# Optimization experiments

Measured on AMD Instinct MI355X. Metric: run time of the kernel, lower is better.

The kernel has to match this reference:

```python
import jax, jax.numpy as jnp
import numpy as np

B, S, D = 8, 2048, 256


def setup_inputs() -> dict:
    key = jax.random.key(0)
    kq, kk, kv, km = jax.random.split(key, 4)
    q = jax.random.normal(kq, (B, S, D), dtype=jnp.float32)
    k = jax.random.normal(kk, (B, S, D), dtype=jnp.float32)
    v = jax.random.normal(kv, (B, S, D), dtype=jnp.float32)
    mask = jax.random.randint(km, (B, S, S), 0, 2, dtype=jnp.int32)
    return {"q": q, "k": k, "v": v, "mask": mask}


def reference(q, k, v, mask):
    d_k = q.shape[-1]
    scale = 1.0 / jnp.sqrt(jnp.float32(d_k))
    # scores: [B, S, S]
    attn = jnp.einsum('bqd,bkd->bqk', q, k) * scale
    attn = jnp.where(mask == 0, jnp.float32(-1e9), attn)
    attn = jax.nn.softmax(attn, axis=-1)
    out = jnp.einsum('bqk,bkd->bqd', attn, v)
    return (out, attn)
```

## Files before the change

### kernel.cpp

```cpp
#include <hip/hip_runtime.h>

constexpr int B = 8, S = 2048, D = 256;
constexpr int TQ = 32;
constexpr float SCALE = 0.0625f;
constexpr int PSTRIDE = 2056;

typedef __attribute__((ext_vector_type(8))) short bf16x8;
typedef __attribute__((ext_vector_type(4))) float f32x4;

__device__ __forceinline__ short f2bf(float f) {
    union { float f; unsigned u; } c; c.f = f;
    unsigned u = c.u + 0x7fffu + ((c.u >> 16) & 1u);
    return (short)(u >> 16);
}

__global__ __launch_bounds__(256) void prepass(
    const float* __restrict__ k, const float* __restrict__ v,
    short* __restrict__ kb, short* __restrict__ vtb)
{
    __shared__ float tile[64][65];
    const int blk = blockIdx.x;
    const int tid = threadIdx.x;

    if (blk < 4096) {
        int i = blk * 256 + tid;
        float4 x = ((const float4*)k)[i];
        short4 o; o.x = f2bf(x.x); o.y = f2bf(x.y); o.z = f2bf(x.z); o.w = f2bf(x.w);
        ((short4*)kb)[i] = o;
    } else {
        int blk2 = blk - 4096;
        int b = blk2 >> 7, rem = blk2 & 127;
        int d0 = (rem & 3) * 64, k0 = (rem >> 2) * 64;
        int tr = tid >> 4, tc = tid & 15;
        const float* vb = v + (size_t)b * S * D;
        #pragma unroll
        for (int r = 0; r < 4; ++r) {
            int key = r * 16 + tr;
            float4 x = *(const float4*)(vb + (size_t)(k0 + key) * D + d0 + tc * 4);
            tile[key][tc * 4 + 0] = x.x; tile[key][tc * 4 + 1] = x.y;
            tile[key][tc * 4 + 2] = x.z; tile[key][tc * 4 + 3] = x.w;
        }
        __syncthreads();
        short* vtbb = vtb + (size_t)b * D * S;
        #pragma unroll
        for (int r = 0; r < 4; ++r) {
            int d = r * 16 + tr;
            short4 o;
            o.x = f2bf(tile[tc * 4 + 0][d]); o.y = f2bf(tile[tc * 4 + 1][d]);
            o.z = f2bf(tile[tc * 4 + 2][d]); o.w = f2bf(tile[tc * 4 + 3][d]);
            *(short4*)(vtbb + (size_t)(d0 + d) * S + k0 + tc * 4) = o;
        }
    }
}

__global__ __launch_bounds__(512, 2) void attn_mfma(
    const float* __restrict__ qf, const short* __restrict__ kb,
    const short* __restrict__ vtb, const int* __restrict__ maskg,
    float* __restrict__ outg, float* __restrict__ attng)
{
    const int b = blockIdx.x & 7;
    const int i0 = (blockIdx.x >> 3) * TQ;
    const int tid = threadIdx.x;
    const int wave = tid >> 6, lane = tid & 63;
    const int quad = lane >> 4, l16 = lane & 15;

    __shared__ short p_lds[TQ][PSTRIDE];
    __shared__ float red[8][TQ];

    bf16x8 aq[2][8];
    const float* qbase = qf + ((size_t)b * S + i0) * D;
    #pragma unroll
    for (int mt = 0; mt < 2; ++mt)
        #pragma unroll
        for (int ks = 0; ks < 8; ++ks) {
            const float* p = qbase + (size_t)(mt * 16 + l16) * D + ks * 32 + quad * 8;
            float4 x0 = *(const float4*)p;
            float4 x1 = *(const float4*)(p + 4);
            bf16x8 a;
            a[0] = f2bf(x0.x); a[1] = f2bf(x0.y); a[2] = f2bf(x0.z); a[3] = f2bf(x0.w);
            a[4] = f2bf(x1.x); a[5] = f2bf(x1.y); a[6] = f2bf(x1.z); a[7] = f2bf(x1.w);
            aq[mt][ks] = a;
        }

    f32x4 acc[2][16];
    #pragma unroll
    for (int mt = 0; mt < 2; ++mt)
        #pragma unroll
        for (int nt = 0; nt < 16; ++nt)
            acc[mt][nt] = f32x4{0.f, 0.f, 0.f, 0.f};

    float rsum[2] = {0.f, 0.f};
    const short* kbase = kb + (size_t)b * S * D;
    const int* mbase0 = maskg + ((size_t)b * S + i0 + l16) * S + wave * 256 + quad * 4;
    const int* mbase1 = mbase0 + (size_t)16 * S;

    #pragma unroll
    for (int nt = 0; nt < 16; ++nt) {
        const int n0 = wave * 256 + nt * 16;
        int4 m0 = *(const int4*)(mbase0 + nt * 16);
        int4 m1 = *(const int4*)(mbase1 + nt * 16);
        bf16x8 bk[8];
        #pragma unroll
        for (int ks = 0; ks < 8; ++ks)
            bk[ks] = *(const bf16x8*)(kbase + (size_t)(n0 + l16) * D + ks * 32 + quad * 8);
        #pragma unroll
        for (int ks = 0; ks < 8; ++ks) {
            acc[0][nt] = __builtin_amdgcn_mfma_f32_16x16x32_bf16(bk[ks], aq[0][ks], acc[0][nt], 0, 0, 0);
            acc[1][nt] = __builtin_amdgcn_mfma_f32_16x16x32_bf16(bk[ks], aq[1][ks], acc[1][nt], 0, 0, 0);
        }
        const int mm0[4] = {m0.x, m0.y, m0.z, m0.w};
        const int mm1[4] = {m1.x, m1.y, m1.z, m1.w};
        #pragma unroll
        for (int r = 0; r < 4; ++r) {
            float e0 = mm0[r] ? __expf(acc[0][nt][r] * SCALE) : 0.0f;
            acc[0][nt][r] = e0; rsum[0] += e0;
            float e1 = mm1[r] ? __expf(acc[1][nt][r] * SCALE) : 0.0f;
            acc[1][nt][r] = e1; rsum[1] += e1;
        }
    }

    #pragma unroll
    for (int mt = 0; mt < 2; ++mt) {
        float v = rsum[mt];
        v += __shfl_xor(v, 16); v += __shfl_xor(v, 32);
        if (quad == 0) red[wave][mt * 16 + l16] = v;
    }
    __syncthreads();

    float inv[2];
    #pragma unroll
    for (int mt = 0; mt < 2; ++mt) {
        float tot = 0.f;
        #pragma unroll
        for (int w = 0; w < 8; ++w) tot += red[w][mt * 16 + l16];
        inv[mt] = 1.0f / tot;
    }

    #pragma unroll
    for (int mt = 0; mt < 2; ++mt) {
        float* arow = attng + ((size_t)b * S + i0 + mt * 16 + l16) * S + wave * 256 + quad * 4;
        #pragma unroll
        for (int nt = 0; nt < 16; ++nt) {
            float4 p4; short4 pb;
            float p0 = acc[mt][nt][0] * inv[mt];
            float p1 = acc[mt][nt][1] * inv[mt];
            float p2 = acc[mt][nt][2] * inv[mt];
            float p3 = acc[mt][nt][3] * inv[mt];
            p4.x = p0; p4.y = p1; p4.z = p2; p4.w = p3;
            pb.x = f2bf(p0); pb.y = f2bf(p1); pb.z = f2bf(p2); pb.w = f2bf(p3);
            *(float4*)(arow + nt * 16) = p4;
            *(short4*)&p_lds[mt * 16 + l16][wave * 256 + nt * 16 + quad * 4] = pb;
        }
    }

    asm volatile("s_waitcnt lgkmcnt(0)" ::: "memory");
    __builtin_amdgcn_s_barrier();
    asm volatile("" ::: "memory");

    f32x4 oacc[2][2];
    #pragma unroll
    for (int mt = 0; mt < 2; ++mt)
        #pragma unroll
        for (int nc = 0; nc < 2; ++nc) oacc[mt][nc] = f32x4{0.f, 0.f, 0.f, 0.f};

    const short* vbase = vtb + (size_t)b * D * S;
    const int nb = wave * 32;
    for (int ks = 0; ks < 64; ++ks) {
        bf16x8 ap[2], bv[2];
        #pragma unroll
        for (int mt = 0; mt < 2; ++mt)
            ap[mt] = *(const bf16x8*)&p_lds[mt * 16 + l16][ks * 32 + quad * 8];
        #pragma unroll
        for (int nc = 0; nc < 2; ++nc)
            bv[nc] = *(const bf16x8*)(vbase + (size_t)(nb + nc * 16 + l16) * S + ks * 32 + quad * 8);
        #pragma unroll
        for (int mt = 0; mt < 2; ++mt)
            #pragma unroll
            for (int nc = 0; nc < 2; ++nc)
                oacc[mt][nc] = __builtin_amdgcn_mfma_f32_16x16x32_bf16(ap[mt], bv[nc], oacc[mt][nc], 0, 0, 0);
    }

    #pragma unroll
    for (int mt = 0; mt < 2; ++mt)
        #pragma unroll
        for (int nc = 0; nc < 2; ++nc)
            #pragma unroll
            for (int r = 0; r < 4; ++r) {
                int row = i0 + mt * 16 + quad * 4 + r;
                int col = nb + nc * 16 + l16;
                outg[((size_t)b * S + row) * D + col] = oacc[mt][nc][r];
            }
}

extern "C" void kernel_launch(void* const* d_in, const int* in_sizes, int n_in,
                              void* d_out, int out_size, void* d_ws, size_t ws_size,
                              hipStream_t stream) {
    const float* q    = (const float*)d_in[0];
    const float* k    = (const float*)d_in[1];
    const float* v    = (const float*)d_in[2];
    const int*   mask = (const int*)d_in[3];
    float* out  = (float*)d_out;
    float* attn = out + (size_t)B * S * D;

    const size_t N = (size_t)B * S * D;
    short* kb  = (short*)d_ws;
    short* vtb = kb + N;

    prepass<<<dim3(5120), 256, 0, stream>>>(k, v, kb, vtb);
    attn_mfma<<<dim3((S / TQ) * B), 512, 0, stream>>>(q, kb, vtb, mask, out, attn);
}
```

Before: 412.6 us.

## Recompute QK^T in a second pass to cut registers and shrink the LDS tile

The large per-wave score accumulator array (32 f32x4) and the full 32x2048 bf16 probability tile in LDS are replaced by a two-pass scheme. The first pass computes QK^T in 256-key chunks, accumulates row sums and packs the mask into 64-bit bitmasks, without keeping the scores. The second pass recomputes QK^T per chunk, normalizes, writes attn, and stages a double-buffered 32x256 bf16 tile in LDS that feeds the PV MFMAs chunk by chunk. This lowers register and LDS use so launch bounds can target 4 blocks per CU, at the cost of doubling the QK^T MFMA work and K reads, plus one barrier per chunk.

```diff
diff --git a/kernel.cpp b/kernel.cpp
--- a/kernel.cpp
+++ b/kernel.cpp
@@ -3,7 +3,7 @@
 constexpr int B = 8, S = 2048, D = 256;
 constexpr int TQ = 32;
 constexpr float SCALE = 0.0625f;
-constexpr int PSTRIDE = 2056;
+constexpr int PST = 264;
 
 typedef __attribute__((ext_vector_type(8))) short bf16x8;
 typedef __attribute__((ext_vector_type(4))) float f32x4;
@@ -53,7 +53,7 @@
     }
 }
 
-__global__ __launch_bounds__(512, 2) void attn_mfma(
+__global__ __launch_bounds__(512, 4) void attn_mfma(
     const float* __restrict__ qf, const short* __restrict__ kb,
     const short* __restrict__ vtb, const int* __restrict__ maskg,
     float* __restrict__ outg, float* __restrict__ attng)
@@ -64,7 +64,7 @@
     const int wave = tid >> 6, lane = tid & 63;
     const int quad = lane >> 4, l16 = lane & 15;
 
-    __shared__ short p_lds[TQ][PSTRIDE];
+    __shared__ short p_lds[2][TQ][PST];
     __shared__ float red[8][TQ];
 
     bf16x8 aq[2][8];
@@ -82,41 +82,51 @@
             aq[mt][ks] = a;
         }
 
-    f32x4 acc[2][16];
-    #pragma unroll
-    for (int mt = 0; mt < 2; ++mt)
-        #pragma unroll
-        for (int nt = 0; nt < 16; ++nt)
-            acc[mt][nt] = f32x4{0.f, 0.f, 0.f, 0.f};
+    const short* kbase = kb + (size_t)b * S * D;
+    const int* mrow0 = maskg + ((size_t)b * S + i0 + l16) * S + quad * 4;
+    const int* mrow1 = mrow0 + (size_t)16 * S;
 
     float rsum[2] = {0.f, 0.f};
-    const short* kbase = kb + (size_t)b * S * D;
-    const int* mbase0 = maskg + ((size_t)b * S + i0 + l16) * S + wave * 256 + quad * 4;
-    const int* mbase1 = mbase0 + (size_t)16 * S;
-
-    #pragma unroll
-    for (int nt = 0; nt < 16; ++nt) {
-        const int n0 = wave * 256 + nt * 16;
-        int4 m0 = *(const int4*)(mbase0 + nt * 16);
-        int4 m1 = *(const int4*)(mbase1 + nt * 16);
-        bf16x8 bk[8];
-        #pragma unroll
-        for (int ks = 0; ks < 8; ++ks)
-            bk[ks] = *(const bf16x8*)(kbase + (size_t)(n0 + l16) * D + ks * 32 + quad * 8);
-        #pragma unroll
-        for (int ks = 0; ks < 8; ++ks) {
-            acc[0][nt] = __builtin_amdgcn_mfma_f32_16x16x32_bf16(bk[ks], aq[0][ks], acc[0][nt], 0, 0, 0);
-            acc[1][nt] = __builtin_amdgcn_mfma_f32_16x16x32_bf16(bk[ks], aq[1][ks], acc[1][nt], 0, 0, 0);
-        }
-        const int mm0[4] = {m0.x, m0.y, m0.z, m0.w};
-        const int mm1[4] = {m1.x, m1.y, m1.z, m1.w};
-        #pragma unroll
-        for (int r = 0; r < 4; ++r) {
-            float e0 = mm0[r] ? __expf(acc[0][nt][r] * SCALE) : 0.0f;
-            acc[0][nt][r] = e0; rsum[0] += e0;
-            float e1 = mm1[r] ? __expf(acc[1][nt][r] * SCALE) : 0.0f;
-            acc[1][nt][r] = e1; rsum[1] += e1;
-        }
+    unsigned long long mb[2] = {0ull, 0ull};
+    #pragma unroll 1
+    for (int t = 0; t < 8; ++t) {
+        const int kq0 = t * 256 + wave * 32;
+        int4 m00 = *(const int4*)(mrow0 + kq0);
+        int4 m01 = *(const int4*)(mrow0 + kq0 + 16);
+        int4 m10 = *(const int4*)(mrow1 + kq0);
+        int4 m11 = *(const int4*)(mrow1 + kq0 + 16);
+        f32x4 acc2[2][2];
+        #pragma unroll
+        for (int mt = 0; mt < 2; ++mt)
+            #pragma unroll
+            for (int nt = 0; nt < 2; ++nt)
+                acc2[mt][nt] = f32x4{0.f, 0.f, 0.f, 0.f};
+        #pragma unroll
+        for (int nt = 0; nt < 2; ++nt) {
+            bf16x8 bk[8];
+            #pragma unroll
+            for (int ks = 0; ks < 8; ++ks)
+                bk[ks] = *(const bf16x8*)(kbase + (size_t)(kq0 + nt * 16 + l16) * D + ks * 32 + quad * 8);
+            #pragma unroll
+            for (int ks = 0; ks < 8; ++ks) {
+                acc2[0][nt] = __builtin_amdgcn_mfma_f32_16x16x32_bf16(bk[ks], aq[0][ks], acc2[0][nt], 0, 0, 0);
+                acc2[1][nt] = __builtin_amdgcn_mfma_f32_16x16x32_bf16(bk[ks], aq[1][ks], acc2[1][nt], 0, 0, 0);
+            }
+        }
+        const int me[2][2][4] = {
+            {{m00.x, m00.y, m00.z, m00.w}, {m01.x, m01.y, m01.z, m01.w}},
+            {{m10.x, m10.y, m10.z, m10.w}, {m11.x, m11.y, m11.z, m11.w}}};
+        #pragma unroll
+        for (int mt = 0; mt < 2; ++mt)
+            #pragma unroll
+            for (int nt = 0; nt < 2; ++nt)
+                #pragma unroll
+                for (int r = 0; r < 4; ++r) {
+                    const bool on = me[mt][nt][r] != 0;
+                    mb[mt] |= (unsigned long long)(on ? 1 : 0) << (t * 8 + nt * 4 + r);
+                    float e = on ? __expf(acc2[mt][nt][r] * SCALE) : 0.0f;
+                    rsum[mt] += e;
+                }
     }
 
     #pragma unroll
@@ -136,27 +146,6 @@
         inv[mt] = 1.0f / tot;
     }
 
-    #pragma unroll
-    for (int mt = 0; mt < 2; ++mt) {
-        float* arow = attng + ((size_t)b * S + i0 + mt * 16 + l16) * S + wave * 256 + quad * 4;
-        #pragma unroll
-        for (int nt = 0; nt < 16; ++nt) {
-            float4 p4; short4 pb;
-            float p0 = acc[mt][nt][0] * inv[mt];
-            float p1 = acc[mt][nt][1] * inv[mt];
-            float p2 = acc[mt][nt][2] * inv[mt];
-            float p3 = acc[mt][nt][3] * inv[mt];
-            p4.x = p0; p4.y = p1; p4.z = p2; p4.w = p3;
-            pb.x = f2bf(p0); pb.y = f2bf(p1); pb.z = f2bf(p2); pb.w = f2bf(p3);
-            *(float4*)(arow + nt * 16) = p4;
-            *(short4*)&p_lds[mt * 16 + l16][wave * 256 + nt * 16 + quad * 4] = pb;
-        }
-    }
-
-    asm volatile("s_waitcnt lgkmcnt(0)" ::: "memory");
-    __builtin_amdgcn_s_barrier();
-    asm volatile("" ::: "memory");
-
     f32x4 oacc[2][2];
     #pragma unroll
     for (int mt = 0; mt < 2; ++mt)
@@ -165,19 +154,60 @@
 
     const short* vbase = vtb + (size_t)b * D * S;
     const int nb = wave * 32;
-    for (int ks = 0; ks < 64; ++ks) {
-        bf16x8 ap[2], bv[2];
+
+    #pragma unroll 1
+    for (int t = 0; t < 8; ++t) {
+        const int kq0 = t * 256 + wave * 32;
+        f32x4 acc2[2][2];
         #pragma unroll
         for (int mt = 0; mt < 2; ++mt)
-            ap[mt] = *(const bf16x8*)&p_lds[mt * 16 + l16][ks * 32 + quad * 8];
-        #pragma unroll
-        for (int nc = 0; nc < 2; ++nc)
-            bv[nc] = *(const bf16x8*)(vbase + (size_t)(nb + nc * 16 + l16) * S + ks * 32 + quad * 8);
-        #pragma unroll
-        for (int mt = 0; mt < 2; ++mt)
-            #pragma unroll
-            for (int nc = 0; nc < 2; ++nc)
-                oacc[mt][nc] = __builtin_amdgcn_mfma_f32_16x16x32_bf16(ap[mt], bv[nc], oacc[mt][nc], 0, 0, 0);
+            #pragma unroll
+            for (int nt = 0; nt < 2; ++nt)
+                acc2[mt][nt] = f32x4{0.f, 0.f, 0.f, 0.f};
+        #pragma unroll
+        for (int nt = 0; nt < 2; ++nt) {
+            bf16x8 bk[8];
+            #pragma unroll
+            for (int ks = 0; ks < 8; ++ks)
+                bk[ks] = *(const bf16x8*)(kbase + (size_t)(kq0 + nt * 16 + l16) * D + ks * 32 + quad * 8);
+            #pragma unroll
+            for (int ks = 0; ks < 8; ++ks) {
+                acc2[0][nt] = __builtin_amdgcn_mfma_f32_16x16x32_bf16(bk[ks], aq[0][ks], acc2[0][nt], 0, 0, 0);
+                acc2[1][nt] = __builtin_amdgcn_mfma_f32_16x16x32_bf16(bk[ks], aq[1][ks], acc2[1][nt], 0, 0, 0);
+            }
+        }
+        #pragma unroll
+        for (int mt = 0; mt < 2; ++mt) {
+            float* arow = attng + ((size_t)b * S + i0 + mt * 16 + l16) * S + kq0 + quad * 4;
+            #pragma unroll
+            for (int nt = 0; nt < 2; ++nt) {
+                float pv[4];
+                #pragma unroll
+                for (int r = 0; r < 4; ++r) {
+                    const bool on = (mb[mt] >> (t * 8 + nt * 4 + r)) & 1ull;
+                    pv[r] = on ? __expf(acc2[mt][nt][r] * SCALE) * inv[mt] : 0.0f;
+                }
+                float4 p4; p4.x = pv[0]; p4.y = pv[1]; p4.z = pv[2]; p4.w = pv[3];
+                short4 pb; pb.x = f2bf(pv[0]); pb.y = f2bf(pv[1]);
+                pb.z = f2bf(pv[2]); pb.w = f2bf(pv[3]);
+                *(float4*)(arow + nt * 16) = p4;
+                *(short4*)&p_lds[t & 1][mt * 16 + l16][wave * 32 + nt * 16 + quad * 4] = pb;
+            }
+        }
+        asm volatile("s_waitcnt lgkmcnt(0)" ::: "memory");
+        __builtin_amdgcn_s_barrier();
+
+        #pragma unroll
+        for (int ks = 0; ks < 8; ++ks) {
+            bf16x8 ap0 = *(const bf16x8*)&p_lds[t & 1][l16][ks * 32 + quad * 8];
+            bf16x8 ap1 = *(const bf16x8*)&p_lds[t & 1][16 + l16][ks * 32 + quad * 8];
+            bf16x8 bv0 = *(const bf16x8*)(vbase + (size_t)(nb + l16) * S + t * 256 + ks * 32 + quad * 8);
+            bf16x8 bv1 = *(const bf16x8*)(vbase + (size_t)(nb + 16 + l16) * S + t * 256 + ks * 32 + quad * 8);
+            oacc[0][0] = __builtin_amdgcn_mfma_f32_16x16x32_bf16(ap0, bv0, oacc[0][0], 0, 0, 0);
+            oacc[0][1] = __builtin_amdgcn_mfma_f32_16x16x32_bf16(ap0, bv1, oacc[0][1], 0, 0, 0);
+            oacc[1][0] = __builtin_amdgcn_mfma_f32_16x16x32_bf16(ap1, bv0, oacc[1][0], 0, 0, 0);
+            oacc[1][1] = __builtin_amdgcn_mfma_f32_16x16x32_bf16(ap1, bv1, oacc[1][1], 0, 0, 0);
+        }
     }
 
     #pragma unroll
```

Measured after the change: 576.0 us. 1.4x slower.

## Split fused attention into scores and PV kernels with atomic row sums

Applied to the files above, without the earlier changes.

Replaces the single fused kernel, in which each block owned 32 query rows across all keys, with two kernels. The first computes masked exp-scores for 32x256 tiles over 4096 blocks, writes unnormalized values to the attn output and accumulates row sums with global atomics. The second reloads those scores, normalizes them, runs the PV matmul and rewrites attn normalized. Q conversion to bf16 and zeroing of the row sums move into the prepass. This exposes far more parallelism and drops the large LDS buffer, at the cost of writing and reading the 128MB attn matrix an extra time.

```diff
diff --git a/kernel.cpp b/kernel.cpp
--- a/kernel.cpp
+++ b/kernel.cpp
@@ -1,9 +1,7 @@
 #include <hip/hip_runtime.h>
 
 constexpr int B = 8, S = 2048, D = 256;
-constexpr int TQ = 32;
 constexpr float SCALE = 0.0625f;
-constexpr int PSTRIDE = 2056;
 
 typedef __attribute__((ext_vector_type(8))) short bf16x8;
 typedef __attribute__((ext_vector_type(4))) float f32x4;
@@ -15,20 +13,24 @@
 }
 
 __global__ __launch_bounds__(256) void prepass(
-    const float* __restrict__ k, const float* __restrict__ v,
-    short* __restrict__ kb, short* __restrict__ vtb)
+    const float* __restrict__ q, const float* __restrict__ k,
+    const float* __restrict__ v,
+    short* __restrict__ qb, short* __restrict__ kb,
+    short* __restrict__ vtb, float* __restrict__ rsumg)
 {
     __shared__ float tile[64][65];
     const int blk = blockIdx.x;
     const int tid = threadIdx.x;
 
-    if (blk < 4096) {
-        int i = blk * 256 + tid;
-        float4 x = ((const float4*)k)[i];
+    if (blk < 8192) {
+        const float* in = (blk < 4096) ? q : k;
+        short* out = (blk < 4096) ? qb : kb;
+        int i = (blk & 4095) * 256 + tid;
+        float4 x = ((const float4*)in)[i];
         short4 o; o.x = f2bf(x.x); o.y = f2bf(x.y); o.z = f2bf(x.z); o.w = f2bf(x.w);
-        ((short4*)kb)[i] = o;
-    } else {
-        int blk2 = blk - 4096;
+        ((short4*)out)[i] = o;
+    } else if (blk < 9216) {
+        int blk2 = blk - 8192;
         int b = blk2 >> 7, rem = blk2 & 127;
         int d0 = (rem & 3) * 64, k0 = (rem >> 2) * 64;
         int tr = tid >> 4, tc = tid & 15;
@@ -50,134 +52,154 @@
             o.z = f2bf(tile[tc * 4 + 2][d]); o.w = f2bf(tile[tc * 4 + 3][d]);
             *(short4*)(vtbb + (size_t)(d0 + d) * S + k0 + tc * 4) = o;
         }
-    }
-}
-
-__global__ __launch_bounds__(512, 2) void attn_mfma(
-    const float* __restrict__ qf, const short* __restrict__ kb,
-    const short* __restrict__ vtb, const int* __restrict__ maskg,
-    float* __restrict__ outg, float* __restrict__ attng)
+    } else {
+        int t = (blk - 9216) * 256 + tid;
+        ((float4*)rsumg)[t] = float4{0.f, 0.f, 0.f, 0.f};
+    }
+}
+
+__global__ __launch_bounds__(512) void attn_scores(
+    const short* __restrict__ qb, const short* __restrict__ kb,
+    const int* __restrict__ maskg, float* __restrict__ attng,
+    float* __restrict__ rsumg)
 {
-    const int b = blockIdx.x & 7;
-    const int i0 = (blockIdx.x >> 3) * TQ;
+    const int blk = blockIdx.x;
+    const int b = blk & 7;
+    const int qt = (blk >> 3) & 63;
+    const int kt = blk >> 9;
+    const int i0 = qt * 32, kq = kt * 256;
     const int tid = threadIdx.x;
     const int wave = tid >> 6, lane = tid & 63;
     const int quad = lane >> 4, l16 = lane & 15;
-
-    __shared__ short p_lds[TQ][PSTRIDE];
-    __shared__ float red[8][TQ];
-
-    bf16x8 aq[2][8];
-    const float* qbase = qf + ((size_t)b * S + i0) * D;
-    #pragma unroll
-    for (int mt = 0; mt < 2; ++mt)
-        #pragma unroll
-        for (int ks = 0; ks < 8; ++ks) {
-            const float* p = qbase + (size_t)(mt * 16 + l16) * D + ks * 32 + quad * 8;
-            float4 x0 = *(const float4*)p;
-            float4 x1 = *(const float4*)(p + 4);
-            bf16x8 a;
-            a[0] = f2bf(x0.x); a[1] = f2bf(x0.y); a[2] = f2bf(x0.z); a[3] = f2bf(x0.w);
-            a[4] = f2bf(x1.x); a[5] = f2bf(x1.y); a[6] = f2bf(x1.z); a[7] = f2bf(x1.w);
-            aq[mt][ks] = a;
-        }
-
-    f32x4 acc[2][16];
-    #pragma unroll
-    for (int mt = 0; mt < 2; ++mt)
-        #pragma unroll
-        for (int nt = 0; nt < 16; ++nt)
+    const int k0w = kq + wave * 32;
+
+    const int* mbase = maskg + ((size_t)b * S + i0 + l16) * S + k0w + quad * 4;
+    int4 m00 = *(const int4*)(mbase);
+    int4 m01 = *(const int4*)(mbase + 16);
+    int4 m10 = *(const int4*)(mbase + (size_t)16 * S);
+    int4 m11 = *(const int4*)(mbase + (size_t)16 * S + 16);
+
+    const short* q0 = qb + ((size_t)b * S + i0 + l16) * D + quad * 8;
+    const short* q1 = q0 + (size_t)16 * D;
+    const short* k0p = kb + ((size_t)b * S + k0w + l16) * D + quad * 8;
+    const short* k1p = k0p + (size_t)16 * D;
+
+    f32x4 acc[2][2];
+    #pragma unroll
+    for (int mt = 0; mt < 2; ++mt)
+        #pragma unroll
+        for (int nt = 0; nt < 2; ++nt)
             acc[mt][nt] = f32x4{0.f, 0.f, 0.f, 0.f};
 
-    float rsum[2] = {0.f, 0.f};
-    const short* kbase = kb + (size_t)b * S * D;
-    const int* mbase0 = maskg + ((size_t)b * S + i0 + l16) * S + wave * 256 + quad * 4;
-    const int* mbase1 = mbase0 + (size_t)16 * S;
-
-    #pragma unroll
-    for (int nt = 0; nt < 16; ++nt) {
-        const int n0 = wave * 256 + nt * 16;
-        int4 m0 = *(const int4*)(mbase0 + nt * 16);
-        int4 m1 = *(const int4*)(mbase1 + nt * 16);
-        bf16x8 bk[8];
-        #pragma unroll
-        for (int ks = 0; ks < 8; ++ks)
-            bk[ks] = *(const bf16x8*)(kbase + (size_t)(n0 + l16) * D + ks * 32 + quad * 8);
-        #pragma unroll
-        for (int ks = 0; ks < 8; ++ks) {
-            acc[0][nt] = __builtin_amdgcn_mfma_f32_16x16x32_bf16(bk[ks], aq[0][ks], acc[0][nt], 0, 0, 0);
-            acc[1][nt] = __builtin_amdgcn_mfma_f32_16x16x32_bf16(bk[ks], aq[1][ks], acc[1][nt], 0, 0, 0);
-        }
-        const int mm0[4] = {m0.x, m0.y, m0.z, m0.w};
-        const int mm1[4] = {m1.x, m1.y, m1.z, m1.w};
-        #pragma unroll
-        for (int r = 0; r < 4; ++r) {
-            float e0 = mm0[r] ? __expf(acc[0][nt][r] * SCALE) : 0.0f;
-            acc[0][nt][r] = e0; rsum[0] += e0;
-            float e1 = mm1[r] ? __expf(acc[1][nt][r] * SCALE) : 0.0f;
-            acc[1][nt][r] = e1; rsum[1] += e1;
-        }
-    }
+    #pragma unroll
+    for (int ks = 0; ks < 8; ++ks) {
+        bf16x8 a0 = *(const bf16x8*)(q0 + ks * 32);
+        bf16x8 a1 = *(const bf16x8*)(q1 + ks * 32);
+        bf16x8 b0 = *(const bf16x8*)(k0p + ks * 32);
+        bf16x8 b1 = *(const bf16x8*)(k1p + ks * 32);
+        acc[0][0] = __builtin_amdgcn_mfma_f32_16x16x32_bf16(b0, a0, acc[0][0], 0, 0, 0);
+        acc[0][1] = __builtin_amdgcn_mfma_f32_16x16x32_bf16(b1, a0, acc[0][1], 0, 0, 0);
+        acc[1][0] = __builtin_amdgcn_mfma_f32_16x16x32_bf16(b0, a1, acc[1][0], 0, 0, 0);
+        acc[1][1] = __builtin_amdgcn_mfma_f32_16x16x32_bf16(b1, a1, acc[1][1], 0, 0, 0);
+    }
+
+    const int mm[2][2][4] = {
+        {{m00.x, m00.y, m00.z, m00.w}, {m01.x, m01.y, m01.z, m01.w}},
+        {{m10.x, m10.y, m10.z, m10.w}, {m11.x, m11.y, m11.z, m11.w}}};
+    float rs[2] = {0.f, 0.f};
+    #pragma unroll
+    for (int mt = 0; mt < 2; ++mt)
+        #pragma unroll
+        for (int nt = 0; nt < 2; ++nt)
+            #pragma unroll
+            for (int r = 0; r < 4; ++r) {
+                float e = mm[mt][nt][r] ? __expf(acc[mt][nt][r] * SCALE) : 0.0f;
+                acc[mt][nt][r] = e;
+                rs[mt] += e;
+            }
 
     #pragma unroll
     for (int mt = 0; mt < 2; ++mt) {
-        float v = rsum[mt];
+        float v = rs[mt];
         v += __shfl_xor(v, 16); v += __shfl_xor(v, 32);
-        if (quad == 0) red[wave][mt * 16 + l16] = v;
-    }
+        if (quad == 0)
+            atomicAdd(rsumg + (size_t)b * S + i0 + mt * 16 + l16, v);
+    }
+
+    #pragma unroll
+    for (int mt = 0; mt < 2; ++mt) {
+        float* arow = attng + ((size_t)b * S + i0 + mt * 16 + l16) * S + k0w + quad * 4;
+        #pragma unroll
+        for (int nt = 0; nt < 2; ++nt) {
+            float4 p4;
+            p4.x = acc[mt][nt][0]; p4.y = acc[mt][nt][1];
+            p4.z = acc[mt][nt][2]; p4.w = acc[mt][nt][3];
+            *(float4*)(arow + nt * 16) = p4;
+        }
+    }
+}
+
+__global__ __launch_bounds__(512) void attn_pv(
+    float* __restrict__ attng, const float* __restrict__ rsumg,
+    const short* __restrict__ vtb, float* __restrict__ outg)
+{
+    const int blk = blockIdx.x;
+    const int b = blk & 7;
+    const int i0 = (blk >> 3) * 32;
+    const int tid = threadIdx.x;
+    const int wave = tid >> 6, lane = tid & 63;
+    const int quad = lane >> 4, l16 = lane & 15;
+
+    float inv[2];
+    inv[0] = 1.0f / rsumg[(size_t)b * S + i0 + l16];
+    inv[1] = 1.0f / rsumg[(size_t)b * S + i0 + 16 + l16];
+
+    f32x4 oacc[2][2];
+    #pragma unroll
+    for (int mt = 0; mt < 2; ++mt)
+        #pragma unroll
+        for (int nc = 0; nc < 2; ++nc) oacc[mt][nc] = f32x4{0.f, 0.f, 0.f, 0.f};
+
+    const short* vbase = vtb + (size_t)b * D * S;
+    const int nb = wave * 32;
+    const float* arow0 = attng + ((size_t)b * S + i0 + l16) * S + quad * 8;
+    const float* arow1 = arow0 + (size_t)16 * S;
+    const short* v0p = vbase + (size_t)(nb + l16) * S + quad * 8;
+    const short* v1p = v0p + (size_t)16 * S;
+
+    for (int ks = 0; ks < 64; ++ks) {
+        float4 pa0a = *(const float4*)(arow0 + ks * 32);
+        float4 pa0b = *(const float4*)(arow0 + ks * 32 + 4);
+        float4 pa1a = *(const float4*)(arow1 + ks * 32);
+        float4 pa1b = *(const float4*)(arow1 + ks * 32 + 4);
+        bf16x8 ap0, ap1;
+        ap0[0] = f2bf(pa0a.x * inv[0]); ap0[1] = f2bf(pa0a.y * inv[0]);
+        ap0[2] = f2bf(pa0a.z * inv[0]); ap0[3] = f2bf(pa0a.w * inv[0]);
+        ap0[4] = f2bf(pa0b.x * inv[0]); ap0[5] = f2bf(pa0b.y * inv[0]);
+        ap0[6] = f2bf(pa0b.z * inv[0]); ap0[7] = f2bf(pa0b.w * inv[0]);
+        ap1[0] = f2bf(pa1a.x * inv[1]); ap1[1] = f2bf(pa1a.y * inv[1]);
+        ap1[2] = f2bf(pa1a.z * inv[1]); ap1[3] = f2bf(pa1a.w * inv[1]);
+        ap1[4] = f2bf(pa1b.x * inv[1]); ap1[5] = f2bf(pa1b.y * inv[1]);
+        ap1[6] = f2bf(pa1b.z * inv[1]); ap1[7] = f2bf(pa1b.w * inv[1]);
+        bf16x8 bv0 = *(const bf16x8*)(v0p + ks * 32);
+        bf16x8 bv1 = *(const bf16x8*)(v1p + ks * 32);
+        oacc[0][0] = __builtin_amdgcn_mfma_f32_16x16x32_bf16(ap0, bv0, oacc[0][0], 0, 0, 0);
+        oacc[0][1] = __builtin_amdgcn_mfma_f32_16x16x32_bf16(ap0, bv1, oacc[0][1], 0, 0, 0);
+        oacc[1][0] = __builtin_amdgcn_mfma_f32_16x16x32_bf16(ap1, bv0, oacc[1][0], 0, 0, 0);
+        oacc[1][1] = __builtin_amdgcn_mfma_f32_16x16x32_bf16(ap1, bv1, oacc[1][1], 0, 0, 0);
+    }
+
     __syncthreads();
-
-    float inv[2];
-    #pragma unroll
-    for (int mt = 0; mt < 2; ++mt) {
-        float tot = 0.f;
-        #pragma unroll
-        for (int w = 0; w < 8; ++w) tot += red[w][mt * 16 + l16];
-        inv[mt] = 1.0f / tot;
-    }
 
     #pragma unroll
     for (int mt = 0; mt < 2; ++mt) {
         float* arow = attng + ((size_t)b * S + i0 + mt * 16 + l16) * S + wave * 256 + quad * 4;
         #pragma unroll
         for (int nt = 0; nt < 16; ++nt) {
-            float4 p4; short4 pb;
-            float p0 = acc[mt][nt][0] * inv[mt];
-            float p1 = acc[mt][nt][1] * inv[mt];
-            float p2 = acc[mt][nt][2] * inv[mt];
-            float p3 = acc[mt][nt][3] * inv[mt];
-            p4.x = p0; p4.y = p1; p4.z = p2; p4.w = p3;
-            pb.x = f2bf(p0); pb.y = f2bf(p1); pb.z = f2bf(p2); pb.w = f2bf(p3);
-            *(float4*)(arow + nt * 16) = p4;
-            *(short4*)&p_lds[mt * 16 + l16][wave * 256 + nt * 16 + quad * 4] = pb;
-        }
-    }
-
-    asm volatile("s_waitcnt lgkmcnt(0)" ::: "memory");
-    __builtin_amdgcn_s_barrier();
-    asm volatile("" ::: "memory");
-
-    f32x4 oacc[2][2];
-    #pragma unroll
-    for (int mt = 0; mt < 2; ++mt)
-        #pragma unroll
-        for (int nc = 0; nc < 2; ++nc) oacc[mt][nc] = f32x4{0.f, 0.f, 0.f, 0.f};
-
-    const short* vbase = vtb + (size_t)b * D * S;
-    const int nb = wave * 32;
-    for (int ks = 0; ks < 64; ++ks) {
-        bf16x8 ap[2], bv[2];
-        #pragma unroll
-        for (int mt = 0; mt < 2; ++mt)
-            ap[mt] = *(const bf16x8*)&p_lds[mt * 16 + l16][ks * 32 + quad * 8];
-        #pragma unroll
-        for (int nc = 0; nc < 2; ++nc)
-            bv[nc] = *(const bf16x8*)(vbase + (size_t)(nb + nc * 16 + l16) * S + ks * 32 + quad * 8);
-        #pragma unroll
-        for (int mt = 0; mt < 2; ++mt)
-            #pragma unroll
-            for (int nc = 0; nc < 2; ++nc)
-                oacc[mt][nc] = __builtin_amdgcn_mfma_f32_16x16x32_bf16(ap[mt], bv[nc], oacc[mt][nc], 0, 0, 0);
+            float4 t = *(const float4*)(arow + nt * 16);
+            t.x *= inv[mt]; t.y *= inv[mt]; t.z *= inv[mt]; t.w *= inv[mt];
+            *(float4*)(arow + nt * 16) = t;
+        }
     }
 
     #pragma unroll
@@ -203,9 +225,12 @@
     float* attn = out + (size_t)B * S * D;
 
     const size_t N = (size_t)B * S * D;
-    short* kb  = (short*)d_ws;
+    short* qb  = (short*)d_ws;
+    short* kb  = qb + N;
     short* vtb = kb + N;
-
-    prepass<<<dim3(5120), 256, 0, stream>>>(k, v, kb, vtb);
-    attn_mfma<<<dim3((S / TQ) * B), 512, 0, stream>>>(q, kb, vtb, mask, out, attn);
-}
+    float* rsumg = (float*)(vtb + N);
+
+    prepass<<<dim3(9232), 256, 0, stream>>>(q, k, v, qb, kb, vtb, rsumg);
+    attn_scores<<<dim3(4096), 512, 0, stream>>>(qb, kb, mask, attn, rsumg);
+    attn_pv<<<dim3(512), 512, 0, stream>>>(attn, rsumg, vtb, out);
+}
```

Result: slower. 597.6 us (+44.8%).
